# Performance work log

Hardware: AMD Instinct MI355X
Metric: run time of the kernel (lower is better)

## Reference

```python
import jax, jax.numpy as jnp
import numpy as np

N_NODES = 50000
N_EDGES = 800000


def setup_inputs() -> dict:
    key = jax.random.key(0)
    ks = jax.random.split(key, 8)
    return {
        "x": jax.random.normal(ks[0], (N_NODES, 256), dtype=jnp.float32),
        "adj_vals": jax.random.uniform(ks[1], (N_EDGES,), dtype=jnp.float32),
        "rows": jax.random.randint(ks[2], (N_EDGES,), 0, N_NODES, dtype=jnp.int32),
        "cols": jax.random.randint(ks[3], (N_EDGES,), 0, N_NODES, dtype=jnp.int32),
        "W1": jax.random.normal(ks[4], (256, 256), dtype=jnp.float32) * (1.0 / np.sqrt(256)),
        "b1": jnp.zeros((256,), dtype=jnp.float32),
        "W2": jax.random.normal(ks[5], (256, 256), dtype=jnp.float32) * (1.0 / np.sqrt(256)),
        "b2": jnp.zeros((256,), dtype=jnp.float32),
        "W3": jax.random.normal(ks[6], (256, 128), dtype=jnp.float32) * (1.0 / np.sqrt(256)),
        "b3": jnp.zeros((128,), dtype=jnp.float32),
    }


def reference(x, adj_vals, rows, cols, W1, b1, W2, b2, W3, b3):
    n = x.shape[0]

    def spmm(h):
        # sparse adjacency matmul: out[r] += val * h[c] over all edges (r, c)
        return jax.ops.segment_sum(adj_vals[:, None] * h[cols], rows, num_segments=n)

    # GCNLayer: adj @ (x @ W) + b ; ReLU between layers (dropout p=0 => identity)
    h = jax.nn.relu(spmm(x @ W1) + b1)
    h = jax.nn.relu(spmm(h @ W2) + b2)
    return spmm(h @ W3) + b3
```

## Files before the change

### kernel.cpp

```cpp
#include <hip/hip_runtime.h>
#include <hip/hip_bf16.h>


#define N_NODES 50000
#define N_EDGES 800000
#define KDIM 256
#define BK 32
#define ELLCAP 64
#define ELLB 782

typedef __attribute__((ext_vector_type(8))) short short8;
typedef __attribute__((ext_vector_type(4))) float f32x4;

__device__ __forceinline__ ushort f2bf(float f) {
    union { float f; unsigned u; } x; x.f = f;
    unsigned r = x.u + 0x7fffu + ((x.u >> 16) & 1u);
    return (ushort)(r >> 16);
}
__device__ __forceinline__ float bf2f(ushort u) {
    union { unsigned u; float f; } x; x.u = ((unsigned)u) << 16;
    return x.f;
}

__device__ __forceinline__ void gld_lds16(const void* g, void* l) {
    __builtin_amdgcn_global_load_lds(
        (const __attribute__((address_space(1))) void*)g,
        (__attribute__((address_space(3))) void*)l, 16, 0, 0);
}

__global__ __launch_bounds__(256) void transpose_all_kernel(
        const float* __restrict__ W1, const float* __restrict__ W2,
        const float* __restrict__ W3, ushort* __restrict__ Wt1,
        ushort* __restrict__ Wt2, ushort* __restrict__ Wt3) {
    int id = blockIdx.x * blockDim.x + threadIdx.x;
    if (id < 65536) {
        int n = id >> 8, k = id & 255;
        Wt1[n * 256 + k] = f2bf(W1[k * 256 + n]);
    } else if (id < 131072) {
        int i = id - 65536, n = i >> 8, k = i & 255;
        Wt2[n * 256 + k] = f2bf(W2[k * 256 + n]);
    } else if (id < 163840) {
        int i = id - 131072, n = i >> 8, k = i & 255;
        Wt3[n * 256 + k] = f2bf(W3[k * 128 + n]);
    }
}


template <bool AFP32>
__device__ __forceinline__ void gemm_body(
        const void* __restrict__ Ain, const ushort* __restrict__ Wt,
        ushort* __restrict__ C, int M, int N, int bx, int by) {
    __shared__ char smem[AFP32 ? 49152 : 32768];
    const int ABYTES = AFP32 ? 16384 : 8192;

    int t = threadIdx.x;
    int lane = t & 63;
    int w = t >> 6;
    int wbase = w * 64;
    int row0 = bx * 128, col0 = by * 128;
    int wm2 = w & 1, wn2 = w >> 1;
    int wm = wm2 * 64, wn = wn2 * 64;
    int q = lane >> 4, mi = lane & 15;

    char* Ab0 = smem;
    char* Ab1 = smem + ABYTES;
    char* Bb0 = smem + 2 * ABYTES;
    char* Bb1 = smem + 2 * ABYTES + 8192;

    const float*  Af = (const float*)Ain;
    const ushort* Au = (const ushort*)Ain;

    auto stageA = [&](char* dst, int k0) {
        if (AFP32) {
            #pragma unroll
            for (int i = 0; i < 4; i++) {
                int D = i * 256 + t;
                int h = D >> 9, s = D & 511;
                int f = s >> 6, lp = s & 63;
                int row = row0 + (f >> 2) * 64 + (f & 3) * 16 + (lp & 15);
                if (row >= M) row = M - 1;
                const float* g = Af + (size_t)row * KDIM + k0 + (lp >> 4) * 8 + h * 4;
                gld_lds16(g, dst + (i * 256 + wbase) * 16);
            }
        } else {
            #pragma unroll
            for (int i = 0; i < 2; i++) {
                int D = i * 256 + t;
                int f = D >> 6, lp = D & 63;
                int row = row0 + (f >> 2) * 64 + (f & 3) * 16 + (lp & 15);
                if (row >= M) row = M - 1;
                const ushort* g = Au + (size_t)row * KDIM + k0 + (lp >> 4) * 8;
                gld_lds16(g, dst + (i * 256 + wbase) * 16);
            }
        }
    };
    auto stageB = [&](char* dst, int k0) {
        #pragma unroll
        for (int i = 0; i < 2; i++) {
            int D = i * 256 + t;
            int f = D >> 6, lp = D & 63;
            int col = col0 + (f >> 2) * 64 + (f & 3) * 16 + (lp & 15);
            const ushort* g = Wt + (size_t)col * KDIM + k0 + (lp >> 4) * 8;
            gld_lds16(g, dst + (i * 256 + wbase) * 16);
        }
    };

    f32x4 acc[4][4];
    #pragma unroll
    for (int i = 0; i < 4; i++)
        #pragma unroll
        for (int j = 0; j < 4; j++) acc[i][j] = (f32x4)0.f;

    stageA(Ab0, 0);
    stageB(Bb0, 0);
    __syncthreads();

    #pragma unroll
    for (int kt = 0; kt < 8; kt++) {
        char* Acur = (kt & 1) ? Ab1 : Ab0;
        char* Bcur = (kt & 1) ? Bb1 : Bb0;
        if (kt < 7) {
            stageA((kt & 1) ? Ab0 : Ab1, (kt + 1) * BK);
            stageB((kt & 1) ? Bb0 : Bb1, (kt + 1) * BK);
        }

        short8 af[4], bfr[4];
        if (AFP32) {
            const float* As = (const float*)Acur;
            #pragma unroll
            for (int mt = 0; mt < 4; mt++) {
                int gA = (wm2 * 4 + mt) * 64 + lane;
                f32x4 lo = *(const f32x4*)(As + gA * 4);
                f32x4 hi = *(const f32x4*)(As + 2048 + gA * 4);
                af[mt][0] = (short)f2bf(lo[0]); af[mt][1] = (short)f2bf(lo[1]);
                af[mt][2] = (short)f2bf(lo[2]); af[mt][3] = (short)f2bf(lo[3]);
                af[mt][4] = (short)f2bf(hi[0]); af[mt][5] = (short)f2bf(hi[1]);
                af[mt][6] = (short)f2bf(hi[2]); af[mt][7] = (short)f2bf(hi[3]);
            }
        } else {
            #pragma unroll
            for (int mt = 0; mt < 4; mt++)
                af[mt] = *(const short8*)(Acur + ((wm2 * 4 + mt) * 64 + lane) * 16);
        }
        #pragma unroll
        for (int nt = 0; nt < 4; nt++)
            bfr[nt] = *(const short8*)(Bcur + ((wn2 * 4 + nt) * 64 + lane) * 16);

        #pragma unroll
        for (int mt = 0; mt < 4; mt++)
            #pragma unroll
            for (int nt = 0; nt < 4; nt++)
                acc[mt][nt] = __builtin_amdgcn_mfma_f32_16x16x32_bf16(
                    af[mt], bfr[nt], acc[mt][nt], 0, 0, 0);

        __syncthreads();
    }

    ushort* Cs = (ushort*)smem;
    #pragma unroll
    for (int mt = 0; mt < 4; mt++)
        #pragma unroll
        for (int r = 0; r < 4; r++)
            #pragma unroll
            for (int nt = 0; nt < 4; nt++)
                Cs[(wm + mt * 16 + q * 4 + r) * 128 + wn + nt * 16 + mi] =
                    f2bf(acc[mt][nt][r]);
    __syncthreads();
    #pragma unroll
    for (int i = 0; i < 8; i++) {
        int idx = i * 256 + t;
        int rr = idx >> 4, gc = idx & 15;
        int grow = row0 + rr;
        if (grow < M)
            *(short8*)&C[(size_t)grow * N + col0 + gc * 8] =
                *(const short8*)&Cs[rr * 128 + gc * 8];
    }
}


__global__ __launch_bounds__(256) void gemm1_ell_kernel(
        const float* __restrict__ x, const ushort* __restrict__ Wt1,
        ushort* __restrict__ C, const int* __restrict__ rows,
        const int* __restrict__ cols, const float* __restrict__ vals,
        int* __restrict__ cnt, int2* __restrict__ cv) {
    int b = blockIdx.x;
    if (b < ELLB) {
        int e0 = (b * 256 + threadIdx.x) * 4;
        if (e0 < N_EDGES) {
            int4   r4 = *(const int4*)&rows[e0];
            int4   c4 = *(const int4*)&cols[e0];
            float4 v4 = *(const float4*)&vals[e0];
            int p0 = atomicAdd(&cnt[r4.x], 1);
            cv[(r4.x << 6) + p0] = make_int2(c4.x, __float_as_int(v4.x));
            int p1 = atomicAdd(&cnt[r4.y], 1);
            cv[(r4.y << 6) + p1] = make_int2(c4.y, __float_as_int(v4.y));
            int p2 = atomicAdd(&cnt[r4.z], 1);
            cv[(r4.z << 6) + p2] = make_int2(c4.z, __float_as_int(v4.z));
            int p3 = atomicAdd(&cnt[r4.w], 1);
            cv[(r4.w << 6) + p3] = make_int2(c4.w, __float_as_int(v4.w));
        }
    } else {
        int g = b - ELLB;
        gemm_body<true>(x, Wt1, C, N_NODES, 256, g % 391, g / 391);
    }
}

template <bool AFP32>
__global__ __launch_bounds__(256) void gemm_bf16_kernel(
        const void* __restrict__ Ain, const ushort* __restrict__ Wt,
        ushort* __restrict__ C, int M, int N) {
    gemm_body<AFP32>(Ain, Wt, C, M, N, blockIdx.x, blockIdx.y);
}


template <int F, bool RELU, bool OUT_BF16>
__global__ __launch_bounds__(256) void spmm_kernel(
        const ushort* __restrict__ H, const int* __restrict__ cnt,
        const int2* __restrict__ cv, const float* __restrict__ bias,
        void* __restrict__ out, int nrows) {
    constexpr int FL = F / 8;
    constexpr int EP = 64 / FL;
    constexpr int STEP = EP * 4;
    int wave = threadIdx.x >> 6, lane = threadIdx.x & 63;
    int r = blockIdx.x * 4 + wave;
    if (r >= nrows) return;
    int fl = lane % FL, ep = lane / FL;
    const ushort* Hl = H + fl * 8;

    float acc[8];
    #pragma unroll
    for (int j = 0; j < 8; j++) acc[j] = 0.f;

    int start = r << 6;
    int end = start + cnt[r];
    for (int base = start; base < end; base += STEP) {
        int e0 = base + ep * 4;
        int2 m0 = cv[e0], m1 = cv[e0 + 1], m2 = cv[e0 + 2], m3 = cv[e0 + 3];
        int   c0 = (e0     < end) ? m0.x : 0;
        int   c1 = (e0 + 1 < end) ? m1.x : 0;
        int   c2 = (e0 + 2 < end) ? m2.x : 0;
        int   c3 = (e0 + 3 < end) ? m3.x : 0;
        float v0 = (e0     < end) ? __int_as_float(m0.y) : 0.f;
        float v1 = (e0 + 1 < end) ? __int_as_float(m1.y) : 0.f;
        float v2 = (e0 + 2 < end) ? __int_as_float(m2.y) : 0.f;
        float v3 = (e0 + 3 < end) ? __int_as_float(m3.y) : 0.f;
        short8 h0 = *(const short8*)&Hl[(size_t)c0 * F];
        short8 h1 = *(const short8*)&Hl[(size_t)c1 * F];
        short8 h2 = *(const short8*)&Hl[(size_t)c2 * F];
        short8 h3 = *(const short8*)&Hl[(size_t)c3 * F];
        #pragma unroll
        for (int j = 0; j < 8; j++)
            acc[j] += v0 * bf2f((ushort)h0[j]) + v1 * bf2f((ushort)h1[j])
                    + v2 * bf2f((ushort)h2[j]) + v3 * bf2f((ushort)h3[j]);
    }

    #pragma unroll
    for (int off = FL; off < 64; off <<= 1)
        #pragma unroll
        for (int j = 0; j < 8; j++) acc[j] += __shfl_down(acc[j], off, 64);

    if (ep == 0) {
        #pragma unroll
        for (int j = 0; j < 8; j++) {
            float o = acc[j] + bias[fl * 8 + j];
            if (RELU) o = fmaxf(o, 0.f);
            acc[j] = o;
        }
        if (OUT_BF16) {
            short8 ob;
            #pragma unroll
            for (int j = 0; j < 8; j++) ob[j] = (short)f2bf(acc[j]);
            *(short8*)((ushort*)out + (size_t)r * F + fl * 8) = ob;
        } else {
            float* of = (float*)out + (size_t)r * F + fl * 8;
            *(float4*)&of[0] = make_float4(acc[0], acc[1], acc[2], acc[3]);
            *(float4*)&of[4] = make_float4(acc[4], acc[5], acc[6], acc[7]);
        }
    }
}


extern "C" void kernel_launch(void* const* d_in, const int* in_sizes, int n_in,
                              void* d_out, int out_size, void* d_ws, size_t ws_size,
                              hipStream_t stream) {
    const float* x    = (const float*)d_in[0];
    const float* av   = (const float*)d_in[1];
    const int*   rows = (const int*)d_in[2];
    const int*   cols = (const int*)d_in[3];
    const float* W1   = (const float*)d_in[4];
    const float* b1   = (const float*)d_in[5];
    const float* W2   = (const float*)d_in[6];
    const float* b2   = (const float*)d_in[7];
    const float* W3   = (const float*)d_in[8];
    const float* b3   = (const float*)d_in[9];
    float* out = (float*)d_out;

    const int N = N_NODES;

    char* p = (char*)d_ws;
    auto carve = [&](size_t bytes) {
        void* q = (void*)p;
        p += (bytes + 255) & ~(size_t)255;
        return q;
    };
    ushort* bufG = (ushort*)carve((size_t)N * 256 * 2);
    ushort* bufH = (ushort*)carve((size_t)N * 256 * 2);
    ushort* Wt1  = (ushort*)carve((size_t)256 * 256 * 2);
    ushort* Wt2  = (ushort*)carve((size_t)256 * 256 * 2);
    ushort* Wt3  = (ushort*)carve((size_t)128 * 256 * 2);
    int*    cnt  = (int*)carve((size_t)N * 4);
    int2*   cv   = (int2*)carve((size_t)N * ELLCAP * 8);

    hipMemsetAsync(cnt, 0, (size_t)N * 4, stream);
    transpose_all_kernel<<<(163840 + 255) / 256, 256, 0, stream>>>(W1, W2, W3, Wt1, Wt2, Wt3);

    gemm1_ell_kernel<<<ELLB + 782, 256, 0, stream>>>(x, Wt1, bufG, rows, cols, av, cnt, cv);

    int spmm_blocks = (N + 3) / 4;
    spmm_kernel<256, true, true><<<spmm_blocks, 256, 0, stream>>>(bufG, cnt, cv, b1, bufH, N);
    gemm_bf16_kernel<false><<<dim3(391, 2), 256, 0, stream>>>(bufH, Wt2, bufG, N, 256);
    spmm_kernel<256, true, true><<<spmm_blocks, 256, 0, stream>>>(bufG, cnt, cv, b2, bufH, N);
    gemm_bf16_kernel<false><<<dim3(391, 1), 256, 0, stream>>>(bufH, Wt3, bufG, N, 128);
    spmm_kernel<128, false, false><<<spmm_blocks, 256, 0, stream>>>(bufG, cnt, cv, b3, out, N);
}
```

Before: 362.7 us.

## Fuse weight transpose with ELL build; widen SpMM edge batch to eight

The weight transpose/bf16 conversion now shares one launch with the ELL adjacency construction, and the first GEMM runs as its own launch instead of being co-launched with the ELL build. The SpMM inner loop processes eight edges per lane per iteration, using 16-byte vector loads of the col/val pairs, which gives more independent gathers in flight. The cv buffer is padded so the wider loads past a row's end stay in bounds. Costs are higher register pressure in SpMM and the loss of overlap between GEMM1 and the atomic ELL build.

```diff
diff --git a/kernel.cpp b/kernel.cpp
--- a/kernel.cpp
+++ b/kernel.cpp
@@ -8,6 +8,7 @@
 #define BK 32
 #define ELLCAP 64
 #define ELLB 782
+#define TRB 640
 
 typedef __attribute__((ext_vector_type(8))) short short8;
 typedef __attribute__((ext_vector_type(4))) float f32x4;
@@ -28,164 +29,28 @@
         (__attribute__((address_space(3))) void*)l, 16, 0, 0);
 }
 
-__global__ __launch_bounds__(256) void transpose_all_kernel(
+__global__ __launch_bounds__(256) void transpose_ell_kernel(
         const float* __restrict__ W1, const float* __restrict__ W2,
         const float* __restrict__ W3, ushort* __restrict__ Wt1,
-        ushort* __restrict__ Wt2, ushort* __restrict__ Wt3) {
-    int id = blockIdx.x * blockDim.x + threadIdx.x;
-    if (id < 65536) {
-        int n = id >> 8, k = id & 255;
-        Wt1[n * 256 + k] = f2bf(W1[k * 256 + n]);
-    } else if (id < 131072) {
-        int i = id - 65536, n = i >> 8, k = i & 255;
-        Wt2[n * 256 + k] = f2bf(W2[k * 256 + n]);
-    } else if (id < 163840) {
-        int i = id - 131072, n = i >> 8, k = i & 255;
-        Wt3[n * 256 + k] = f2bf(W3[k * 128 + n]);
-    }
-}
-
-
-template <bool AFP32>
-__device__ __forceinline__ void gemm_body(
-        const void* __restrict__ Ain, const ushort* __restrict__ Wt,
-        ushort* __restrict__ C, int M, int N, int bx, int by) {
-    __shared__ char smem[AFP32 ? 49152 : 32768];
-    const int ABYTES = AFP32 ? 16384 : 8192;
-
-    int t = threadIdx.x;
-    int lane = t & 63;
-    int w = t >> 6;
-    int wbase = w * 64;
-    int row0 = bx * 128, col0 = by * 128;
-    int wm2 = w & 1, wn2 = w >> 1;
-    int wm = wm2 * 64, wn = wn2 * 64;
-    int q = lane >> 4, mi = lane & 15;
-
-    char* Ab0 = smem;
-    char* Ab1 = smem + ABYTES;
-    char* Bb0 = smem + 2 * ABYTES;
-    char* Bb1 = smem + 2 * ABYTES + 8192;
-
-    const float*  Af = (const float*)Ain;
-    const ushort* Au = (const ushort*)Ain;
-
-    auto stageA = [&](char* dst, int k0) {
-        if (AFP32) {
-            #pragma unroll
-            for (int i = 0; i < 4; i++) {
-                int D = i * 256 + t;
-                int h = D >> 9, s = D & 511;
-                int f = s >> 6, lp = s & 63;
-                int row = row0 + (f >> 2) * 64 + (f & 3) * 16 + (lp & 15);
-                if (row >= M) row = M - 1;
-                const float* g = Af + (size_t)row * KDIM + k0 + (lp >> 4) * 8 + h * 4;
-                gld_lds16(g, dst + (i * 256 + wbase) * 16);
-            }
+        ushort* __restrict__ Wt2, ushort* __restrict__ Wt3,
+        const int* __restrict__ rows, const int* __restrict__ cols,
+        const float* __restrict__ vals, int* __restrict__ cnt,
+        int2* __restrict__ cv) {
+    int b = blockIdx.x;
+    if (b < TRB) {
+        int id = b * 256 + threadIdx.x;
+        if (id < 65536) {
+            int n = id >> 8, k = id & 255;
+            Wt1[n * 256 + k] = f2bf(W1[k * 256 + n]);
+        } else if (id < 131072) {
+            int i = id - 65536, n = i >> 8, k = i & 255;
+            Wt2[n * 256 + k] = f2bf(W2[k * 256 + n]);
         } else {
-            #pragma unroll
-            for (int i = 0; i < 2; i++) {
-                int D = i * 256 + t;
-                int f = D >> 6, lp = D & 63;
-                int row = row0 + (f >> 2) * 64 + (f & 3) * 16 + (lp & 15);
-                if (row >= M) row = M - 1;
-                const ushort* g = Au + (size_t)row * KDIM + k0 + (lp >> 4) * 8;
-                gld_lds16(g, dst + (i * 256 + wbase) * 16);
-            }
-        }
-    };
-    auto stageB = [&](char* dst, int k0) {
-        #pragma unroll
-        for (int i = 0; i < 2; i++) {
-            int D = i * 256 + t;
-            int f = D >> 6, lp = D & 63;
-            int col = col0 + (f >> 2) * 64 + (f & 3) * 16 + (lp & 15);
-            const ushort* g = Wt + (size_t)col * KDIM + k0 + (lp >> 4) * 8;
-            gld_lds16(g, dst + (i * 256 + wbase) * 16);
-        }
-    };
-
-    f32x4 acc[4][4];
-    #pragma unroll
-    for (int i = 0; i < 4; i++)
-        #pragma unroll
-        for (int j = 0; j < 4; j++) acc[i][j] = (f32x4)0.f;
-
-    stageA(Ab0, 0);
-    stageB(Bb0, 0);
-    __syncthreads();
-
-    #pragma unroll
-    for (int kt = 0; kt < 8; kt++) {
-        char* Acur = (kt & 1) ? Ab1 : Ab0;
-        char* Bcur = (kt & 1) ? Bb1 : Bb0;
-        if (kt < 7) {
-            stageA((kt & 1) ? Ab0 : Ab1, (kt + 1) * BK);
-            stageB((kt & 1) ? Bb0 : Bb1, (kt + 1) * BK);
-        }
-
-        short8 af[4], bfr[4];
-        if (AFP32) {
-            const float* As = (const float*)Acur;
-            #pragma unroll
-            for (int mt = 0; mt < 4; mt++) {
-                int gA = (wm2 * 4 + mt) * 64 + lane;
-                f32x4 lo = *(const f32x4*)(As + gA * 4);
-                f32x4 hi = *(const f32x4*)(As + 2048 + gA * 4);
-                af[mt][0] = (short)f2bf(lo[0]); af[mt][1] = (short)f2bf(lo[1]);
-                af[mt][2] = (short)f2bf(lo[2]); af[mt][3] = (short)f2bf(lo[3]);
-                af[mt][4] = (short)f2bf(hi[0]); af[mt][5] = (short)f2bf(hi[1]);
-                af[mt][6] = (short)f2bf(hi[2]); af[mt][7] = (short)f2bf(hi[3]);
-            }
-        } else {
-            #pragma unroll
-            for (int mt = 0; mt < 4; mt++)
-                af[mt] = *(const short8*)(Acur + ((wm2 * 4 + mt) * 64 + lane) * 16);
-        }
-        #pragma unroll
-        for (int nt = 0; nt < 4; nt++)
-            bfr[nt] = *(const short8*)(Bcur + ((wn2 * 4 + nt) * 64 + lane) * 16);
-
-        #pragma unroll
-        for (int mt = 0; mt < 4; mt++)
-            #pragma unroll
-            for (int nt = 0; nt < 4; nt++)
-                acc[mt][nt] = __builtin_amdgcn_mfma_f32_16x16x32_bf16(
-                    af[mt], bfr[nt], acc[mt][nt], 0, 0, 0);
-
-        __syncthreads();
-    }
-
-    ushort* Cs = (ushort*)smem;
-    #pragma unroll
-    for (int mt = 0; mt < 4; mt++)
-        #pragma unroll
-        for (int r = 0; r < 4; r++)
-            #pragma unroll
-            for (int nt = 0; nt < 4; nt++)
-                Cs[(wm + mt * 16 + q * 4 + r) * 128 + wn + nt * 16 + mi] =
-                    f2bf(acc[mt][nt][r]);
-    __syncthreads();
-    #pragma unroll
-    for (int i = 0; i < 8; i++) {
-        int idx = i * 256 + t;
-        int rr = idx >> 4, gc = idx & 15;
-        int grow = row0 + rr;
-        if (grow < M)
-            *(short8*)&C[(size_t)grow * N + col0 + gc * 8] =
-                *(const short8*)&Cs[rr * 128 + gc * 8];
-    }
-}
-
-
-__global__ __launch_bounds__(256) void gemm1_ell_kernel(
-        const float* __restrict__ x, const ushort* __restrict__ Wt1,
-        ushort* __restrict__ C, const int* __restrict__ rows,
-        const int* __restrict__ cols, const float* __restrict__ vals,
-        int* __restrict__ cnt, int2* __restrict__ cv) {
-    int b = blockIdx.x;
-    if (b < ELLB) {
-        int e0 = (b * 256 + threadIdx.x) * 4;
+            int i = id - 131072, n = i >> 8, k = i & 255;
+            Wt3[n * 256 + k] = f2bf(W3[k * 128 + n]);
+        }
+    } else {
+        int e0 = ((b - TRB) * 256 + threadIdx.x) * 4;
         if (e0 < N_EDGES) {
             int4   r4 = *(const int4*)&rows[e0];
             int4   c4 = *(const int4*)&cols[e0];
@@ -199,9 +64,138 @@
             int p3 = atomicAdd(&cnt[r4.w], 1);
             cv[(r4.w << 6) + p3] = make_int2(c4.w, __float_as_int(v4.w));
         }
-    } else {
-        int g = b - ELLB;
-        gemm_body<true>(x, Wt1, C, N_NODES, 256, g % 391, g / 391);
+    }
+}
+
+
+template <bool AFP32>
+__device__ __forceinline__ void gemm_body(
+        const void* __restrict__ Ain, const ushort* __restrict__ Wt,
+        ushort* __restrict__ C, int M, int N, int bx, int by) {
+    __shared__ char smem[AFP32 ? 49152 : 32768];
+    const int ABYTES = AFP32 ? 16384 : 8192;
+
+    int t = threadIdx.x;
+    int lane = t & 63;
+    int w = t >> 6;
+    int wbase = w * 64;
+    int row0 = bx * 128, col0 = by * 128;
+    int wm2 = w & 1, wn2 = w >> 1;
+    int wm = wm2 * 64, wn = wn2 * 64;
+    int q = lane >> 4, mi = lane & 15;
+
+    char* Ab0 = smem;
+    char* Ab1 = smem + ABYTES;
+    char* Bb0 = smem + 2 * ABYTES;
+    char* Bb1 = smem + 2 * ABYTES + 8192;
+
+    const float*  Af = (const float*)Ain;
+    const ushort* Au = (const ushort*)Ain;
+
+    auto stageA = [&](char* dst, int k0) {
+        if (AFP32) {
+            #pragma unroll
+            for (int i = 0; i < 4; i++) {
+                int D = i * 256 + t;
+                int h = D >> 9, s = D & 511;
+                int f = s >> 6, lp = s & 63;
+                int row = row0 + (f >> 2) * 64 + (f & 3) * 16 + (lp & 15);
+                if (row >= M) row = M - 1;
+                const float* g = Af + (size_t)row * KDIM + k0 + (lp >> 4) * 8 + h * 4;
+                gld_lds16(g, dst + (i * 256 + wbase) * 16);
+            }
+        } else {
+            #pragma unroll
+            for (int i = 0; i < 2; i++) {
+                int D = i * 256 + t;
+                int f = D >> 6, lp = D & 63;
+                int row = row0 + (f >> 2) * 64 + (f & 3) * 16 + (lp & 15);
+                if (row >= M) row = M - 1;
+                const ushort* g = Au + (size_t)row * KDIM + k0 + (lp >> 4) * 8;
+                gld_lds16(g, dst + (i * 256 + wbase) * 16);
+            }
+        }
+    };
+    auto stageB = [&](char* dst, int k0) {
+        #pragma unroll
+        for (int i = 0; i < 2; i++) {
+            int D = i * 256 + t;
+            int f = D >> 6, lp = D & 63;
+            int col = col0 + (f >> 2) * 64 + (f & 3) * 16 + (lp & 15);
+            const ushort* g = Wt + (size_t)col * KDIM + k0 + (lp >> 4) * 8;
+            gld_lds16(g, dst + (i * 256 + wbase) * 16);
+        }
+    };
+
+    f32x4 acc[4][4];
+    #pragma unroll
+    for (int i = 0; i < 4; i++)
+        #pragma unroll
+        for (int j = 0; j < 4; j++) acc[i][j] = (f32x4)0.f;
+
+    stageA(Ab0, 0);
+    stageB(Bb0, 0);
+    __syncthreads();
+
+    #pragma unroll
+    for (int kt = 0; kt < 8; kt++) {
+        char* Acur = (kt & 1) ? Ab1 : Ab0;
+        char* Bcur = (kt & 1) ? Bb1 : Bb0;
+        if (kt < 7) {
+            stageA((kt & 1) ? Ab0 : Ab1, (kt + 1) * BK);
+            stageB((kt & 1) ? Bb0 : Bb1, (kt + 1) * BK);
+        }
+
+        short8 af[4], bfr[4];
+        if (AFP32) {
+            const float* As = (const float*)Acur;
+            #pragma unroll
+            for (int mt = 0; mt < 4; mt++) {
+                int gA = (wm2 * 4 + mt) * 64 + lane;
+                f32x4 lo = *(const f32x4*)(As + gA * 4);
+                f32x4 hi = *(const f32x4*)(As + 2048 + gA * 4);
+                af[mt][0] = (short)f2bf(lo[0]); af[mt][1] = (short)f2bf(lo[1]);
+                af[mt][2] = (short)f2bf(lo[2]); af[mt][3] = (short)f2bf(lo[3]);
+                af[mt][4] = (short)f2bf(hi[0]); af[mt][5] = (short)f2bf(hi[1]);
+                af[mt][6] = (short)f2bf(hi[2]); af[mt][7] = (short)f2bf(hi[3]);
+            }
+        } else {
+            #pragma unroll
+            for (int mt = 0; mt < 4; mt++)
+                af[mt] = *(const short8*)(Acur + ((wm2 * 4 + mt) * 64 + lane) * 16);
+        }
+        #pragma unroll
+        for (int nt = 0; nt < 4; nt++)
+            bfr[nt] = *(const short8*)(Bcur + ((wn2 * 4 + nt) * 64 + lane) * 16);
+
+        #pragma unroll
+        for (int mt = 0; mt < 4; mt++)
+            #pragma unroll
+            for (int nt = 0; nt < 4; nt++)
+                acc[mt][nt] = __builtin_amdgcn_mfma_f32_16x16x32_bf16(
+                    af[mt], bfr[nt], acc[mt][nt], 0, 0, 0);
+
+        __syncthreads();
+    }
+
+    ushort* Cs = (ushort*)smem;
+    #pragma unroll
+    for (int mt = 0; mt < 4; mt++)
+        #pragma unroll
+        for (int r = 0; r < 4; r++)
+            #pragma unroll
+            for (int nt = 0; nt < 4; nt++)
+                Cs[(wm + mt * 16 + q * 4 + r) * 128 + wn + nt * 16 + mi] =
+                    f2bf(acc[mt][nt][r]);
+    __syncthreads();
+    #pragma unroll
+    for (int i = 0; i < 8; i++) {
+        int idx = i * 256 + t;
+        int rr = idx >> 4, gc = idx & 15;
+        int grow = row0 + rr;
+        if (grow < M)
+            *(short8*)&C[(size_t)grow * N + col0 + gc * 8] =
+                *(const short8*)&Cs[rr * 128 + gc * 8];
     }
 }
 
@@ -220,7 +214,7 @@
         void* __restrict__ out, int nrows) {
     constexpr int FL = F / 8;
     constexpr int EP = 64 / FL;
-    constexpr int STEP = EP * 4;
+    constexpr int STEP = EP * 8;
     int wave = threadIdx.x >> 6, lane = threadIdx.x & 63;
     int r = blockIdx.x * 4 + wave;
     if (r >= nrows) return;
@@ -234,24 +228,35 @@
     int start = r << 6;
     int end = start + cnt[r];
     for (int base = start; base < end; base += STEP) {
-        int e0 = base + ep * 4;
-        int2 m0 = cv[e0], m1 = cv[e0 + 1], m2 = cv[e0 + 2], m3 = cv[e0 + 3];
-        int   c0 = (e0     < end) ? m0.x : 0;
-        int   c1 = (e0 + 1 < end) ? m1.x : 0;
-        int   c2 = (e0 + 2 < end) ? m2.x : 0;
-        int   c3 = (e0 + 3 < end) ? m3.x : 0;
-        float v0 = (e0     < end) ? __int_as_float(m0.y) : 0.f;
-        float v1 = (e0 + 1 < end) ? __int_as_float(m1.y) : 0.f;
-        float v2 = (e0 + 2 < end) ? __int_as_float(m2.y) : 0.f;
-        float v3 = (e0 + 3 < end) ? __int_as_float(m3.y) : 0.f;
-        short8 h0 = *(const short8*)&Hl[(size_t)c0 * F];
-        short8 h1 = *(const short8*)&Hl[(size_t)c1 * F];
-        short8 h2 = *(const short8*)&Hl[(size_t)c2 * F];
-        short8 h3 = *(const short8*)&Hl[(size_t)c3 * F];
-        #pragma unroll
-        for (int j = 0; j < 8; j++)
-            acc[j] += v0 * bf2f((ushort)h0[j]) + v1 * bf2f((ushort)h1[j])
-                    + v2 * bf2f((ushort)h2[j]) + v3 * bf2f((ushort)h3[j]);
+        int e0 = base + ep * 8;
+        int4 ma = *(const int4*)&cv[e0];
+        int4 mb = *(const int4*)&cv[e0 + 2];
+        int4 mc = *(const int4*)&cv[e0 + 4];
+        int4 md = *(const int4*)&cv[e0 + 6];
+        int   c[8];
+        float v[8];
+        c[0] = ma.x; v[0] = __int_as_float(ma.y);
+        c[1] = ma.z; v[1] = __int_as_float(ma.w);
+        c[2] = mb.x; v[2] = __int_as_float(mb.y);
+        c[3] = mb.z; v[3] = __int_as_float(mb.w);
+        c[4] = mc.x; v[4] = __int_as_float(mc.y);
+        c[5] = mc.z; v[5] = __int_as_float(mc.w);
+        c[6] = md.x; v[6] = __int_as_float(md.y);
+        c[7] = md.z; v[7] = __int_as_float(md.w);
+        #pragma unroll
+        for (int u = 0; u < 8; u++) {
+            if (e0 + u >= end) { c[u] = 0; v[u] = 0.f; }
+        }
+        short8 h[8];
+        #pragma unroll
+        for (int u = 0; u < 8; u++)
+            h[u] = *(const short8*)&Hl[(size_t)c[u] * F];
+        #pragma unroll
+        for (int j = 0; j < 8; j++) {
+            #pragma unroll
+            for (int u = 0; u < 8; u++)
+                acc[j] += v[u] * bf2f((ushort)h[u][j]);
+        }
     }
 
     #pragma unroll
@@ -309,12 +314,14 @@
     ushort* Wt2  = (ushort*)carve((size_t)256 * 256 * 2);
     ushort* Wt3  = (ushort*)carve((size_t)128 * 256 * 2);
     int*    cnt  = (int*)carve((size_t)N * 4);
-    int2*   cv   = (int2*)carve((size_t)N * ELLCAP * 8);
+    int2*   cv   = (int2*)carve(((size_t)N * ELLCAP + 128) * 8);
 
     hipMemsetAsync(cnt, 0, (size_t)N * 4, stream);
-    transpose_all_kernel<<<(163840 + 255) / 256, 256, 0, stream>>>(W1, W2, W3, Wt1, Wt2, Wt3);
-
-    gemm1_ell_kernel<<<ELLB + 782, 256, 0, stream>>>(x, Wt1, bufG, rows, cols, av, cnt, cv);
+
+    transpose_ell_kernel<<<TRB + ELLB, 256, 0, stream>>>(
+        W1, W2, W3, Wt1, Wt2, Wt3, rows, cols, av, cnt, cv);
+
+    gemm_bf16_kernel<true><<<dim3(391, 2), 256, 0, stream>>>(x, Wt1, bufG, N, 256);
 
     int spmm_blocks = (N + 3) / 4;
     spmm_kernel<256, true, true><<<spmm_blocks, 256, 0, stream>>>(bufG, cnt, cv, b1, bufH, N);
```

Result: no change. 362.2 us (-0.1%).
